# Kernel optimization log

Hardware: AMD Instinct MI355X
Metric: run time of the kernel (lower is better)

## Reference

```python
import jax, jax.numpy as jnp
import numpy as np

D_MODEL = 512
DK = 4
DV = 8
HIDD = 10
HEAD = D_MODEL // DV  # 64
LN_EPS = 1e-5


def setup_inputs() -> dict:
    key = jax.random.key(0)
    ks = jax.random.split(key, 10)
    B, S, Se = 8, 512, 512
    u = jax.random.uniform  # torch.rand initializer for attention weights
    n = jax.random.normal
    return {
        "x": n(ks[0], (B, S, D_MODEL), jnp.float32),
        "x_enc": n(ks[1], (B, Se, D_MODEL), jnp.float32),
        "WqM": u(ks[2], (D_MODEL, HEAD * DK), jnp.float32),
        "WkM": u(ks[3], (D_MODEL, HEAD * DK), jnp.float32),
        "WvM": u(ks[4], (D_MODEL, HEAD * DV), jnp.float32),
        "ln_g": jnp.ones((D_MODEL,), jnp.float32),
        "ln_b": jnp.zeros((D_MODEL,), jnp.float32),
        "fc1_w": n(ks[5], (HIDD, D_MODEL), jnp.float32) * (1.0 / np.sqrt(D_MODEL)),
        "fc1_b": jnp.zeros((HIDD,), jnp.float32),
        "fc2_w": n(ks[6], (D_MODEL, HIDD), jnp.float32) * (1.0 / np.sqrt(HIDD)),
        "fc2_b": jnp.zeros((D_MODEL,), jnp.float32),
    }


def _attention(Xq, Xkv, WqM, WkM, WvM, causal_mul_mask):
    # NOTE: cross-attention in the source also uses WqM/WkM/WvM (Wq/Wk/Wv unused).
    B, Sq, _ = Xq.shape
    Sk = Xkv.shape[1]
    Q = (Xq @ WqM).reshape(B, Sq, HEAD, DK)
    K = (Xkv @ WkM).reshape(B, Sk, HEAD, DK)
    V = (Xkv @ WvM).reshape(B, Sk, HEAD, DV)
    score = jnp.einsum('bqhd,bkhd->bhqk', Q, K) / np.sqrt(DK).astype(np.float32)
    if causal_mul_mask:
        # Faithful quirk: multiplicative tril mask on scores (NOT additive -inf).
        score = score * jnp.tril(jnp.ones((Sq, Sk), score.dtype))
    w = jax.nn.softmax(score, axis=-1)
    out = jnp.einsum('bhqk,bkhd->bqhd', w, V)
    return out.reshape(B, Sq, HEAD * DV)  # HEAD*DV == d_model


def _layernorm(x, g, b):
    mu = jnp.mean(x, axis=-1, keepdims=True)
    var = jnp.mean(jnp.square(x - mu), axis=-1, keepdims=True)
    return (x - mu) * jax.lax.rsqrt(var + LN_EPS) * g + b


def reference(x, x_enc, WqM, WkM, WvM, ln_g, ln_b, fc1_w, fc1_b, fc2_w, fc2_b):
    fx = _attention(x, x, WqM, WkM, WvM, causal_mul_mask=True)
    fx = _attention(fx, x_enc, WqM, WkM, WvM, causal_mul_mask=False)
    y = _layernorm(x + fx, ln_g, ln_b)
    h = jax.nn.relu(y @ fc1_w.T + fc1_b)
    return h @ fc2_w.T + fc2_b
```

## Files before the change

kernel.cpp:

```cpp
#include <hip/hip_runtime.h>
#include <math.h>

#define D_MODEL 512
#define BATCH 8
#define SEQ 512
#define HEAD 64
#define DK 4
#define DV 8
#define HIDD 10

#define MR 32
#define KC 32
#define NC 256

__global__ __launch_bounds__(256) void proj_kernel(
    const float* __restrict__ xq, const float* __restrict__ xkv,
    const float* __restrict__ Wq, const float* __restrict__ Wk,
    const float* __restrict__ Wv,
    float* __restrict__ Q2, float* __restrict__ K2, float* __restrict__ V2)
{
    __shared__ float xt[KC * MR];
    __shared__ float wt[KC * NC];

    const int t  = threadIdx.x;
    const int bj = blockIdx.x & 3;
    const int br = blockIdx.x >> 2;
    const int r0 = br * MR;

    const float* X; const float* W; int ldw; int c0;
    if (bj == 0)      { X = xq;  W = Wq; ldw = 256; c0 = 0;   }
    else if (bj == 1) { X = xkv; W = Wk; ldw = 256; c0 = 0;   }
    else if (bj == 2) { X = xkv; W = Wv; ldw = 512; c0 = 0;   }
    else              { X = xkv; W = Wv; ldw = 512; c0 = 256; }

    const int rg = t >> 6;
    const int cq = t & 63;
    const int rs = t & 31;
    const int kq = t >> 5;

    float4 acc[8];
#pragma unroll
    for (int r = 0; r < 8; ++r) acc[r] = make_float4(0.f, 0.f, 0.f, 0.f);

    for (int kc = 0; kc < D_MODEL; kc += KC) {
        const float4 xa = *(const float4*)(X + (long)(r0 + rs) * D_MODEL + kc + kq * 4);
        xt[(kq * 4 + 0) * MR + rs] = xa.x;
        xt[(kq * 4 + 1) * MR + rs] = xa.y;
        xt[(kq * 4 + 2) * MR + rs] = xa.z;
        xt[(kq * 4 + 3) * MR + rs] = xa.w;

#pragma unroll
        for (int i = 0; i < 8; ++i) {
            const int row = i * 4 + rg;
            *(float4*)(wt + row * NC + cq * 4) =
                *(const float4*)(W + (long)(kc + row) * ldw + c0 + cq * 4);
        }
        __syncthreads();

#pragma unroll 4
        for (int k = 0; k < KC; ++k) {
            const float4 w4 = *(const float4*)(wt + k * NC + cq * 4);
            const float4 x0 = *(const float4*)(xt + k * MR + rg * 8);
            const float4 x1 = *(const float4*)(xt + k * MR + rg * 8 + 4);
            const float xr[8] = {x0.x, x0.y, x0.z, x0.w, x1.x, x1.y, x1.z, x1.w};
#pragma unroll
            for (int r = 0; r < 8; ++r) {
                acc[r].x = fmaf(xr[r], w4.x, acc[r].x);
                acc[r].y = fmaf(xr[r], w4.y, acc[r].y);
                acc[r].z = fmaf(xr[r], w4.z, acc[r].z);
                acc[r].w = fmaf(xr[r], w4.w, acc[r].w);
            }
        }
        __syncthreads();
    }

    const int b = r0 >> 9;
    const int sb = (r0 & 511) + rg * 8;
    if (bj <= 1) {
        float* dst = (bj == 0) ? Q2 : K2;
#pragma unroll
        for (int r = 0; r < 8; ++r)
            *(float4*)(dst + (((long)b * HEAD + cq) * SEQ + sb + r) * 4) = acc[r];
    } else {
        const int col = c0 + cq * 4;
        const int h = col >> 3;
        const int off = col & 7;
#pragma unroll
        for (int r = 0; r < 8; ++r)
            *(float4*)(V2 + (((long)b * HEAD + h) * SEQ + sb + r) * 8 + off) = acc[r];
    }
}

__global__ __launch_bounds__(256) void attn_kernel(
    const float* __restrict__ Q2, const float* __restrict__ K2,
    const float* __restrict__ V2, float* __restrict__ O, int causal)
{
    extern __shared__ float smem[];
    float* Kl = smem;
    float* Vl = smem + SEQ * DK;
    float* cs = Vl + SEQ * DV;

    const int t = threadIdx.x;
    const int bh = blockIdx.x >> 1;
    const int qhalf = blockIdx.x & 1;
    const int b = bh >> 6;
    const int h = bh & 63;

    const float4* Ks = (const float4*)(K2 + (long)bh * SEQ * DK);
    ((float4*)Kl)[t]       = Ks[t];
    ((float4*)Kl)[t + 256] = Ks[t + 256];
    const float4* Vs = (const float4*)(V2 + (long)bh * SEQ * DV);
#pragma unroll
    for (int i = 0; i < 4; ++i)
        ((float4*)Vl)[t + i * 256] = Vs[t + i * 256];
    __syncthreads();

    if (causal) {
        const int ch = t >> 3, d = t & 7;
        float s16 = 0.f;
#pragma unroll
        for (int i = 0; i < 16; ++i) s16 += Vl[(ch * 16 + i) * 8 + d];
        cs[ch * 8 + d] = s16;
        __syncthreads();
        if (t < 8) {
            cs[256 + t] = 0.f;
            float run = 0.f;
            for (int c2 = 31; c2 >= 0; --c2) {
                run += cs[c2 * 8 + t];
                cs[c2 * 8 + t] = run;
            }
        }
        __syncthreads();
    }

    const int q = qhalf * 256 + t;
    const float4 qv = *(const float4*)(Q2 + ((long)bh * SEQ + q) * 4);
    const float q0 = qv.x * 0.5f, q1 = qv.y * 0.5f;
    const float q2 = qv.z * 0.5f, q3 = qv.w * 0.5f;

    const int bound = causal ? q : (SEQ - 1);

    float m = -INFINITY, l = 0.f;
    float a0=0.f,a1=0.f,a2=0.f,a3=0.f,a4=0.f,a5=0.f,a6=0.f,a7=0.f;

    int s0 = 0;
    for (; s0 + 8 <= bound + 1; s0 += 8) {
        float sc[8];
#pragma unroll
        for (int i = 0; i < 8; ++i) {
            const float4 k4 = *(const float4*)(Kl + (s0 + i) * 4);
            sc[i] = fmaf(q0, k4.x, fmaf(q1, k4.y, fmaf(q2, k4.z, q3 * k4.w)));
        }
        float gm = fmaxf(fmaxf(fmaxf(sc[0], sc[1]), fmaxf(sc[2], sc[3])),
                         fmaxf(fmaxf(sc[4], sc[5]), fmaxf(sc[6], sc[7])));
        if (gm > m) {
            float scale = __expf(m - gm);
            l *= scale;
            a0*=scale; a1*=scale; a2*=scale; a3*=scale;
            a4*=scale; a5*=scale; a6*=scale; a7*=scale;
            m = gm;
        }
#pragma unroll
        for (int i = 0; i < 8; ++i) {
            float p = __expf(sc[i] - m);
            l += p;
            const float4 v0 = *(const float4*)(Vl + (s0 + i) * 8);
            const float4 v1 = *(const float4*)(Vl + (s0 + i) * 8 + 4);
            a0 = fmaf(p, v0.x, a0); a1 = fmaf(p, v0.y, a1);
            a2 = fmaf(p, v0.z, a2); a3 = fmaf(p, v0.w, a3);
            a4 = fmaf(p, v1.x, a4); a5 = fmaf(p, v1.y, a5);
            a6 = fmaf(p, v1.z, a6); a7 = fmaf(p, v1.w, a7);
        }
    }
    for (int s = s0; s <= bound; ++s) {
        const float4 k4 = *(const float4*)(Kl + s * 4);
        float sc = fmaf(q0, k4.x, fmaf(q1, k4.y, fmaf(q2, k4.z, q3 * k4.w)));
        if (sc > m) {
            float scale = __expf(m - sc);
            l *= scale;
            a0*=scale; a1*=scale; a2*=scale; a3*=scale;
            a4*=scale; a5*=scale; a6*=scale; a7*=scale;
            m = sc;
        }
        float p = __expf(sc - m);
        l += p;
        const float4 v0 = *(const float4*)(Vl + s * 8);
        const float4 v1 = *(const float4*)(Vl + s * 8 + 4);
        a0 = fmaf(p, v0.x, a0); a1 = fmaf(p, v0.y, a1);
        a2 = fmaf(p, v0.z, a2); a3 = fmaf(p, v0.w, a3);
        a4 = fmaf(p, v1.x, a4); a5 = fmaf(p, v1.y, a5);
        a6 = fmaf(p, v1.z, a6); a7 = fmaf(p, v1.w, a7);
    }

    if (causal && q < SEQ - 1) {
        float M = fmaxf(m, 0.f);
        float scale = __expf(m - M);
        float pm = __expf(-M);
        l = l * scale + pm * (float)(SEQ - 1 - q);
        int nq = q + 1;
        int cq2 = nq >> 4;
        float sv[8];
#pragma unroll
        for (int d = 0; d < 8; ++d) sv[d] = cs[(cq2 + 1) * 8 + d];
        for (int s = nq; s < (cq2 + 1) * 16; ++s) {
            const float4 v0 = *(const float4*)(Vl + s * 8);
            const float4 v1 = *(const float4*)(Vl + s * 8 + 4);
            sv[0]+=v0.x; sv[1]+=v0.y; sv[2]+=v0.z; sv[3]+=v0.w;
            sv[4]+=v1.x; sv[5]+=v1.y; sv[6]+=v1.z; sv[7]+=v1.w;
        }
        a0 = a0*scale + pm*sv[0]; a1 = a1*scale + pm*sv[1];
        a2 = a2*scale + pm*sv[2]; a3 = a3*scale + pm*sv[3];
        a4 = a4*scale + pm*sv[4]; a5 = a5*scale + pm*sv[5];
        a6 = a6*scale + pm*sv[6]; a7 = a7*scale + pm*sv[7];
    }

    float inv = 1.0f / l;
    const long obase = (long)b * SEQ * 512 + (long)q * 512 + h * DV;
    *(float4*)(O + obase)     = make_float4(a0*inv, a1*inv, a2*inv, a3*inv);
    *(float4*)(O + obase + 4) = make_float4(a4*inv, a5*inv, a6*inv, a7*inv);
}

__global__ __launch_bounds__(256) void ln_mlp_kernel(
    const float* __restrict__ x, const float* __restrict__ fx,
    const float* __restrict__ g, const float* __restrict__ beta,
    const float* __restrict__ w1, const float* __restrict__ b1,
    const float* __restrict__ w2, const float* __restrict__ b2,
    float* __restrict__ out)
{
    const int t = threadIdx.x;
    const int lane = t & 63;
    const int row = blockIdx.x * 4 + (t >> 6);
    const long base = (long)row * D_MODEL;
    const int e0 = lane * 8;

    const float4 xa = *(const float4*)(x + base + e0);
    const float4 xb = *(const float4*)(x + base + e0 + 4);
    const float4 fa = *(const float4*)(fx + base + e0);
    const float4 fb = *(const float4*)(fx + base + e0 + 4);
    float z[8] = {xa.x+fa.x, xa.y+fa.y, xa.z+fa.z, xa.w+fa.w,
                  xb.x+fb.x, xb.y+fb.y, xb.z+fb.z, xb.w+fb.w};

    float sum = 0.f;
#pragma unroll
    for (int j = 0; j < 8; ++j) sum += z[j];
#pragma unroll
    for (int o = 32; o > 0; o >>= 1) sum += __shfl_xor(sum, o);
    float mu = sum * (1.0f / 512.0f);

    float d[8], ss = 0.f;
#pragma unroll
    for (int j = 0; j < 8; ++j) { d[j] = z[j] - mu; ss += d[j] * d[j]; }
#pragma unroll
    for (int o = 32; o > 0; o >>= 1) ss += __shfl_xor(ss, o);
    float rs = rsqrtf(ss * (1.0f / 512.0f) + 1e-5f);

    const float4 ga = *(const float4*)(g + e0);
    const float4 gb = *(const float4*)(g + e0 + 4);
    const float4 ba = *(const float4*)(beta + e0);
    const float4 bb = *(const float4*)(beta + e0 + 4);
    const float gg[8] = {ga.x,ga.y,ga.z,ga.w,gb.x,gb.y,gb.z,gb.w};
    const float bt[8] = {ba.x,ba.y,ba.z,ba.w,bb.x,bb.y,bb.z,bb.w};
    float y[8];
#pragma unroll
    for (int j = 0; j < 8; ++j) y[j] = d[j] * rs * gg[j] + bt[j];

    float part[HIDD];
#pragma unroll
    for (int i = 0; i < HIDD; ++i) {
        const float4 wa = *(const float4*)(w1 + i * 512 + e0);
        const float4 wb = *(const float4*)(w1 + i * 512 + e0 + 4);
        part[i] = y[0]*wa.x + y[1]*wa.y + y[2]*wa.z + y[3]*wa.w
                + y[4]*wb.x + y[5]*wb.y + y[6]*wb.z + y[7]*wb.w;
    }
#pragma unroll
    for (int i = 0; i < HIDD; ++i)
#pragma unroll
        for (int o = 32; o > 0; o >>= 1) part[i] += __shfl_xor(part[i], o);

    float hv[HIDD];
#pragma unroll
    for (int i = 0; i < HIDD; ++i) hv[i] = fmaxf(part[i] + b1[i], 0.f);

    float o8[8];
#pragma unroll
    for (int j = 0; j < 8; ++j) o8[j] = b2[e0 + j];
#pragma unroll
    for (int i = 0; i < HIDD; ++i)
#pragma unroll
        for (int j = 0; j < 8; ++j)
            o8[j] = fmaf(hv[i], w2[(long)(e0 + j) * 10 + i], o8[j]);

    *(float4*)(out + base + e0)     = make_float4(o8[0], o8[1], o8[2], o8[3]);
    *(float4*)(out + base + e0 + 4) = make_float4(o8[4], o8[5], o8[6], o8[7]);
}

extern "C" void kernel_launch(void* const* d_in, const int* in_sizes, int n_in,
                              void* d_out, int out_size, void* d_ws, size_t ws_size,
                              hipStream_t stream) {
    (void)in_sizes; (void)n_in; (void)out_size; (void)ws_size;
    const float* x    = (const float*)d_in[0];
    const float* xenc = (const float*)d_in[1];
    const float* Wq   = (const float*)d_in[2];
    const float* Wk   = (const float*)d_in[3];
    const float* Wv   = (const float*)d_in[4];
    const float* ln_g = (const float*)d_in[5];
    const float* ln_b = (const float*)d_in[6];
    const float* w1   = (const float*)d_in[7];
    const float* b1   = (const float*)d_in[8];
    const float* w2   = (const float*)d_in[9];
    const float* b2   = (const float*)d_in[10];
    float* out = (float*)d_out;

    float* ws = (float*)d_ws;
    float* Q2 = ws;
    float* K2 = Q2 + 1048576;
    float* V2 = K2 + 1048576;
    float* A  = V2 + 2097152;

    const int nrows = BATCH * SEQ;
    const size_t lds_cross  = (size_t)(SEQ * DK + SEQ * DV) * 4;
    const size_t lds_causal = lds_cross + (size_t)(33 * DV) * 4;
    const int proj_grid = (nrows / MR) * 4;

    proj_kernel<<<dim3(proj_grid), 256, 0, stream>>>(x, x, Wq, Wk, Wv, Q2, K2, V2);
    attn_kernel<<<dim3(BATCH * HEAD * 2), 256, lds_causal, stream>>>(Q2, K2, V2, A, 1);

    proj_kernel<<<dim3(proj_grid), 256, 0, stream>>>(A, xenc, Wq, Wk, Wv, Q2, K2, V2);
    attn_kernel<<<dim3(BATCH * HEAD * 2), 256, lds_cross, stream>>>(Q2, K2, V2, A, 0);

    ln_mlp_kernel<<<dim3(nrows / 4), 256, 0, stream>>>(x, A, ln_g, ln_b,
                                                       w1, b1, w2, b2, out);
}
```

Baseline: 340.8 us.

## Rewrite projection and attention kernels with global-memory weights and simpler causal loop

The projection kernel is retiled so each block handles 64 rows by 64 output columns, with only X staged in padded shared memory and weights read directly from global memory (relying on cache broadcast). The attention kernel drops shared-memory staging of K/V and the prefix-sum shortcut for the multiplicative causal mask. It now runs the full 512-key loop with masked scores set to zero and is templated on causality. This removes shared-memory traffic and syncs, but doubles the causal attention work and relies on L1/L2 for the K/V and weight reads.

```diff
diff --git a/kernel.cpp b/kernel.cpp
--- a/kernel.cpp
+++ b/kernel.cpp
@@ -9,9 +9,8 @@
 #define DV 8
 #define HIDD 10
 
-#define MR 32
-#define KC 32
-#define NC 256
+#define KC 128
+#define XPAD 129
 
 __global__ __launch_bounds__(256) void proj_kernel(
     const float* __restrict__ xq, const float* __restrict__ xkv,
@@ -19,205 +18,142 @@
     const float* __restrict__ Wv,
     float* __restrict__ Q2, float* __restrict__ K2, float* __restrict__ V2)
 {
-    __shared__ float xt[KC * MR];
-    __shared__ float wt[KC * NC];
+    __shared__ float xt[64 * XPAD];
 
     const int t  = threadIdx.x;
-    const int bj = blockIdx.x & 3;
-    const int br = blockIdx.x >> 2;
-    const int r0 = br * MR;
-
-    const float* X; const float* W; int ldw; int c0;
-    if (bj == 0)      { X = xq;  W = Wq; ldw = 256; c0 = 0;   }
-    else if (bj == 1) { X = xkv; W = Wk; ldw = 256; c0 = 0;   }
-    else if (bj == 2) { X = xkv; W = Wv; ldw = 512; c0 = 0;   }
-    else              { X = xkv; W = Wv; ldw = 512; c0 = 256; }
-
-    const int rg = t >> 6;
-    const int cq = t & 63;
-    const int rs = t & 31;
-    const int kq = t >> 5;
-
-    float4 acc[8];
-#pragma unroll
-    for (int r = 0; r < 8; ++r) acc[r] = make_float4(0.f, 0.f, 0.f, 0.f);
+    const int cj = blockIdx.x & 15;
+    const int br = blockIdx.x >> 4;
+    const int r0 = br * 64;
+
+    const float* X; const float* W; int ldw, c0, which;
+    if (cj < 4)      { X = xq;  W = Wq; ldw = 256; c0 = cj * 64;       which = 0; }
+    else if (cj < 8) { X = xkv; W = Wk; ldw = 256; c0 = (cj - 4) * 64; which = 1; }
+    else             { X = xkv; W = Wv; ldw = 512; c0 = (cj - 8) * 64; which = 2; }
+
+    const int lane = t & 63;
+    const int wv   = t >> 6;
+    const int cw   = c0 + wv * 16;
+
+    float acc[16];
+#pragma unroll
+    for (int c = 0; c < 16; ++c) acc[c] = 0.f;
 
     for (int kc = 0; kc < D_MODEL; kc += KC) {
-        const float4 xa = *(const float4*)(X + (long)(r0 + rs) * D_MODEL + kc + kq * 4);
-        xt[(kq * 4 + 0) * MR + rs] = xa.x;
-        xt[(kq * 4 + 1) * MR + rs] = xa.y;
-        xt[(kq * 4 + 2) * MR + rs] = xa.z;
-        xt[(kq * 4 + 3) * MR + rs] = xa.w;
-
+        __syncthreads();
 #pragma unroll
         for (int i = 0; i < 8; ++i) {
-            const int row = i * 4 + rg;
-            *(float4*)(wt + row * NC + cq * 4) =
-                *(const float4*)(W + (long)(kc + row) * ldw + c0 + cq * 4);
+            const int slot = t + i * 256;
+            const int row  = slot >> 5;
+            const int c4   = (slot & 31) * 4;
+            const float4 v = *(const float4*)(X + (long)(r0 + row) * D_MODEL + kc + c4);
+            xt[row * XPAD + c4 + 0] = v.x;
+            xt[row * XPAD + c4 + 1] = v.y;
+            xt[row * XPAD + c4 + 2] = v.z;
+            xt[row * XPAD + c4 + 3] = v.w;
         }
         __syncthreads();
 
 #pragma unroll 4
         for (int k = 0; k < KC; ++k) {
-            const float4 w4 = *(const float4*)(wt + k * NC + cq * 4);
-            const float4 x0 = *(const float4*)(xt + k * MR + rg * 8);
-            const float4 x1 = *(const float4*)(xt + k * MR + rg * 8 + 4);
-            const float xr[8] = {x0.x, x0.y, x0.z, x0.w, x1.x, x1.y, x1.z, x1.w};
-#pragma unroll
-            for (int r = 0; r < 8; ++r) {
-                acc[r].x = fmaf(xr[r], w4.x, acc[r].x);
-                acc[r].y = fmaf(xr[r], w4.y, acc[r].y);
-                acc[r].z = fmaf(xr[r], w4.z, acc[r].z);
-                acc[r].w = fmaf(xr[r], w4.w, acc[r].w);
-            }
-        }
-        __syncthreads();
+            const float* wr = W + (long)(kc + k) * ldw + cw;
+            const float4 w0 = *(const float4*)(wr);
+            const float4 w1 = *(const float4*)(wr + 4);
+            const float4 w2 = *(const float4*)(wr + 8);
+            const float4 w3 = *(const float4*)(wr + 12);
+            const float xv = xt[lane * XPAD + k];
+            acc[0]  = fmaf(xv, w0.x, acc[0]);  acc[1]  = fmaf(xv, w0.y, acc[1]);
+            acc[2]  = fmaf(xv, w0.z, acc[2]);  acc[3]  = fmaf(xv, w0.w, acc[3]);
+            acc[4]  = fmaf(xv, w1.x, acc[4]);  acc[5]  = fmaf(xv, w1.y, acc[5]);
+            acc[6]  = fmaf(xv, w1.z, acc[6]);  acc[7]  = fmaf(xv, w1.w, acc[7]);
+            acc[8]  = fmaf(xv, w2.x, acc[8]);  acc[9]  = fmaf(xv, w2.y, acc[9]);
+            acc[10] = fmaf(xv, w2.z, acc[10]); acc[11] = fmaf(xv, w2.w, acc[11]);
+            acc[12] = fmaf(xv, w3.x, acc[12]); acc[13] = fmaf(xv, w3.y, acc[13]);
+            acc[14] = fmaf(xv, w3.z, acc[14]); acc[15] = fmaf(xv, w3.w, acc[15]);
+        }
     }
 
     const int b = r0 >> 9;
-    const int sb = (r0 & 511) + rg * 8;
-    if (bj <= 1) {
-        float* dst = (bj == 0) ? Q2 : K2;
-#pragma unroll
-        for (int r = 0; r < 8; ++r)
-            *(float4*)(dst + (((long)b * HEAD + cq) * SEQ + sb + r) * 4) = acc[r];
+    const int s = (r0 & 511) + lane;
+    if (which <= 1) {
+        float* dst = (which == 0) ? Q2 : K2;
+#pragma unroll
+        for (int hh = 0; hh < 4; ++hh) {
+            const int h = (cw >> 2) + hh;
+            *(float4*)(dst + (((long)b * HEAD + h) * SEQ + s) * 4) =
+                make_float4(acc[hh*4+0], acc[hh*4+1], acc[hh*4+2], acc[hh*4+3]);
+        }
     } else {
-        const int col = c0 + cq * 4;
-        const int h = col >> 3;
-        const int off = col & 7;
-#pragma unroll
-        for (int r = 0; r < 8; ++r)
-            *(float4*)(V2 + (((long)b * HEAD + h) * SEQ + sb + r) * 8 + off) = acc[r];
-    }
-}
-
+#pragma unroll
+        for (int hh = 0; hh < 2; ++hh) {
+            const int h = (cw >> 3) + hh;
+            const long vb = (((long)b * HEAD + h) * SEQ + s) * 8;
+            *(float4*)(V2 + vb)     = make_float4(acc[hh*8+0], acc[hh*8+1],
+                                                  acc[hh*8+2], acc[hh*8+3]);
+            *(float4*)(V2 + vb + 4) = make_float4(acc[hh*8+4], acc[hh*8+5],
+                                                  acc[hh*8+6], acc[hh*8+7]);
+        }
+    }
+}
+
+template <int CAUSAL>
 __global__ __launch_bounds__(256) void attn_kernel(
     const float* __restrict__ Q2, const float* __restrict__ K2,
-    const float* __restrict__ V2, float* __restrict__ O, int causal)
+    const float* __restrict__ V2, float* __restrict__ O)
 {
-    extern __shared__ float smem[];
-    float* Kl = smem;
-    float* Vl = smem + SEQ * DK;
-    float* cs = Vl + SEQ * DV;
-
-    const int t = threadIdx.x;
+    const int t  = threadIdx.x;
+    const int qh = blockIdx.x & 1;
     const int bh = blockIdx.x >> 1;
-    const int qhalf = blockIdx.x & 1;
-    const int b = bh >> 6;
-    const int h = bh & 63;
-
-    const float4* Ks = (const float4*)(K2 + (long)bh * SEQ * DK);
-    ((float4*)Kl)[t]       = Ks[t];
-    ((float4*)Kl)[t + 256] = Ks[t + 256];
-    const float4* Vs = (const float4*)(V2 + (long)bh * SEQ * DV);
-#pragma unroll
-    for (int i = 0; i < 4; ++i)
-        ((float4*)Vl)[t + i * 256] = Vs[t + i * 256];
-    __syncthreads();
-
-    if (causal) {
-        const int ch = t >> 3, d = t & 7;
-        float s16 = 0.f;
-#pragma unroll
-        for (int i = 0; i < 16; ++i) s16 += Vl[(ch * 16 + i) * 8 + d];
-        cs[ch * 8 + d] = s16;
-        __syncthreads();
-        if (t < 8) {
-            cs[256 + t] = 0.f;
-            float run = 0.f;
-            for (int c2 = 31; c2 >= 0; --c2) {
-                run += cs[c2 * 8 + t];
-                cs[c2 * 8 + t] = run;
-            }
-        }
-        __syncthreads();
-    }
-
-    const int q = qhalf * 256 + t;
+    const int b  = bh >> 6;
+    const int h  = bh & 63;
+
+    const int q = qh * 256 + t;
     const float4 qv = *(const float4*)(Q2 + ((long)bh * SEQ + q) * 4);
     const float q0 = qv.x * 0.5f, q1 = qv.y * 0.5f;
     const float q2 = qv.z * 0.5f, q3 = qv.w * 0.5f;
 
-    const int bound = causal ? q : (SEQ - 1);
+    const float* Kp = K2 + (long)bh * SEQ * DK;
+    const float* Vp = V2 + (long)bh * SEQ * DV;
 
     float m = -INFINITY, l = 0.f;
-    float a0=0.f,a1=0.f,a2=0.f,a3=0.f,a4=0.f,a5=0.f,a6=0.f,a7=0.f;
-
-    int s0 = 0;
-    for (; s0 + 8 <= bound + 1; s0 += 8) {
+    float A[8];
+#pragma unroll
+    for (int d = 0; d < 8; ++d) A[d] = 0.f;
+
+    for (int s0 = 0; s0 < SEQ; s0 += 8) {
         float sc[8];
 #pragma unroll
         for (int i = 0; i < 8; ++i) {
-            const float4 k4 = *(const float4*)(Kl + (s0 + i) * 4);
-            sc[i] = fmaf(q0, k4.x, fmaf(q1, k4.y, fmaf(q2, k4.z, q3 * k4.w)));
-        }
-        float gm = fmaxf(fmaxf(fmaxf(sc[0], sc[1]), fmaxf(sc[2], sc[3])),
-                         fmaxf(fmaxf(sc[4], sc[5]), fmaxf(sc[6], sc[7])));
+            const float4 k4 = *(const float4*)(Kp + (s0 + i) * 4);
+            float v = fmaf(q0, k4.x, fmaf(q1, k4.y, fmaf(q2, k4.z, q3 * k4.w)));
+            if (CAUSAL) v = (s0 + i <= q) ? v : 0.f;
+            sc[i] = v;
+        }
+        const float gm = fmaxf(fmaxf(fmaxf(sc[0], sc[1]), fmaxf(sc[2], sc[3])),
+                               fmaxf(fmaxf(sc[4], sc[5]), fmaxf(sc[6], sc[7])));
         if (gm > m) {
-            float scale = __expf(m - gm);
-            l *= scale;
-            a0*=scale; a1*=scale; a2*=scale; a3*=scale;
-            a4*=scale; a5*=scale; a6*=scale; a7*=scale;
+            const float r = __expf(m - gm);
+            l *= r;
+#pragma unroll
+            for (int d = 0; d < 8; ++d) A[d] *= r;
             m = gm;
         }
 #pragma unroll
         for (int i = 0; i < 8; ++i) {
-            float p = __expf(sc[i] - m);
+            const float p = __expf(sc[i] - m);
             l += p;
-            const float4 v0 = *(const float4*)(Vl + (s0 + i) * 8);
-            const float4 v1 = *(const float4*)(Vl + (s0 + i) * 8 + 4);
-            a0 = fmaf(p, v0.x, a0); a1 = fmaf(p, v0.y, a1);
-            a2 = fmaf(p, v0.z, a2); a3 = fmaf(p, v0.w, a3);
-            a4 = fmaf(p, v1.x, a4); a5 = fmaf(p, v1.y, a5);
-            a6 = fmaf(p, v1.z, a6); a7 = fmaf(p, v1.w, a7);
-        }
-    }
-    for (int s = s0; s <= bound; ++s) {
-        const float4 k4 = *(const float4*)(Kl + s * 4);
-        float sc = fmaf(q0, k4.x, fmaf(q1, k4.y, fmaf(q2, k4.z, q3 * k4.w)));
-        if (sc > m) {
-            float scale = __expf(m - sc);
-            l *= scale;
-            a0*=scale; a1*=scale; a2*=scale; a3*=scale;
-            a4*=scale; a5*=scale; a6*=scale; a7*=scale;
-            m = sc;
-        }
-        float p = __expf(sc - m);
-        l += p;
-        const float4 v0 = *(const float4*)(Vl + s * 8);
-        const float4 v1 = *(const float4*)(Vl + s * 8 + 4);
-        a0 = fmaf(p, v0.x, a0); a1 = fmaf(p, v0.y, a1);
-        a2 = fmaf(p, v0.z, a2); a3 = fmaf(p, v0.w, a3);
-        a4 = fmaf(p, v1.x, a4); a5 = fmaf(p, v1.y, a5);
-        a6 = fmaf(p, v1.z, a6); a7 = fmaf(p, v1.w, a7);
-    }
-
-    if (causal && q < SEQ - 1) {
-        float M = fmaxf(m, 0.f);
-        float scale = __expf(m - M);
-        float pm = __expf(-M);
-        l = l * scale + pm * (float)(SEQ - 1 - q);
-        int nq = q + 1;
-        int cq2 = nq >> 4;
-        float sv[8];
-#pragma unroll
-        for (int d = 0; d < 8; ++d) sv[d] = cs[(cq2 + 1) * 8 + d];
-        for (int s = nq; s < (cq2 + 1) * 16; ++s) {
-            const float4 v0 = *(const float4*)(Vl + s * 8);
-            const float4 v1 = *(const float4*)(Vl + s * 8 + 4);
-            sv[0]+=v0.x; sv[1]+=v0.y; sv[2]+=v0.z; sv[3]+=v0.w;
-            sv[4]+=v1.x; sv[5]+=v1.y; sv[6]+=v1.z; sv[7]+=v1.w;
-        }
-        a0 = a0*scale + pm*sv[0]; a1 = a1*scale + pm*sv[1];
-        a2 = a2*scale + pm*sv[2]; a3 = a3*scale + pm*sv[3];
-        a4 = a4*scale + pm*sv[4]; a5 = a5*scale + pm*sv[5];
-        a6 = a6*scale + pm*sv[6]; a7 = a7*scale + pm*sv[7];
-    }
-
-    float inv = 1.0f / l;
-    const long obase = (long)b * SEQ * 512 + (long)q * 512 + h * DV;
-    *(float4*)(O + obase)     = make_float4(a0*inv, a1*inv, a2*inv, a3*inv);
-    *(float4*)(O + obase + 4) = make_float4(a4*inv, a5*inv, a6*inv, a7*inv);
+            const float4 v0 = *(const float4*)(Vp + (s0 + i) * 8);
+            const float4 v1 = *(const float4*)(Vp + (s0 + i) * 8 + 4);
+            A[0] = fmaf(p, v0.x, A[0]); A[1] = fmaf(p, v0.y, A[1]);
+            A[2] = fmaf(p, v0.z, A[2]); A[3] = fmaf(p, v0.w, A[3]);
+            A[4] = fmaf(p, v1.x, A[4]); A[5] = fmaf(p, v1.y, A[5]);
+            A[6] = fmaf(p, v1.z, A[6]); A[7] = fmaf(p, v1.w, A[7]);
+        }
+    }
+
+    const float inv = 1.0f / l;
+    const long ob = ((long)b * SEQ + q) * 512 + h * DV;
+    *(float4*)(O + ob)     = make_float4(A[0]*inv, A[1]*inv, A[2]*inv, A[3]*inv);
+    *(float4*)(O + ob + 4) = make_float4(A[4]*inv, A[5]*inv, A[6]*inv, A[7]*inv);
 }
 
 __global__ __launch_bounds__(256) void ln_mlp_kernel(
@@ -317,17 +253,12 @@
     float* V2 = K2 + 1048576;
     float* A  = V2 + 2097152;
 
-    const int nrows = BATCH * SEQ;
-    const size_t lds_cross  = (size_t)(SEQ * DK + SEQ * DV) * 4;
-    const size_t lds_causal = lds_cross + (size_t)(33 * DV) * 4;
-    const int proj_grid = (nrows / MR) * 4;
-
-    proj_kernel<<<dim3(proj_grid), 256, 0, stream>>>(x, x, Wq, Wk, Wv, Q2, K2, V2);
-    attn_kernel<<<dim3(BATCH * HEAD * 2), 256, lds_causal, stream>>>(Q2, K2, V2, A, 1);
-
-    proj_kernel<<<dim3(proj_grid), 256, 0, stream>>>(A, xenc, Wq, Wk, Wv, Q2, K2, V2);
-    attn_kernel<<<dim3(BATCH * HEAD * 2), 256, lds_cross, stream>>>(Q2, K2, V2, A, 0);
-
-    ln_mlp_kernel<<<dim3(nrows / 4), 256, 0, stream>>>(x, A, ln_g, ln_b,
-                                                       w1, b1, w2, b2, out);
-}
+    proj_kernel<<<dim3(1024), 256, 0, stream>>>(x, x, Wq, Wk, Wv, Q2, K2, V2);
+    attn_kernel<1><<<dim3(BATCH * HEAD * 2), 256, 0, stream>>>(Q2, K2, V2, A);
+
+    proj_kernel<<<dim3(1024), 256, 0, stream>>>(A, xenc, Wq, Wk, Wv, Q2, K2, V2);
+    attn_kernel<0><<<dim3(BATCH * HEAD * 2), 256, 0, stream>>>(Q2, K2, V2, A);
+
+    ln_mlp_kernel<<<dim3(BATCH * SEQ / 4), 256, 0, stream>>>(x, A, ln_g, ln_b,
+                                                             w1, b1, w2, b2, out);
+}
```

Measured after the change: 742.5 us. +117.9%, slower.
